# Optimization experiments

Hardware: AMD Instinct MI355X
Metric: run time of the kernel (lower is better)

## Reference

```python
import jax, jax.numpy as jnp
import numpy as np

A = 4096          # agents
N_OBJ = 8192      # objects
IN_DIM = 16       # input_dim
EMBED = 128       # embedding_dim
MAX_OBJ = 16      # max set size
DEG = 8           # communicate in-degree (constant, target-major edges)
OBS_DEG = 8       # observe degree
POS_DIM = 2
ORIG = IN_DIM + POS_DIM   # 18, decoded element dim
THRES = 0.02              # duplicate filter distance threshold


def setup_inputs() -> dict:
    key = jax.random.key(0)
    ks = jax.random.split(key, 16)
    def lin(k, fi, fo):
        return (jax.random.normal(k, (fi, fo), jnp.float32) / np.float32(np.sqrt(fi)))
    obj_x = jax.random.normal(ks[0], (N_OBJ, IN_DIM), jnp.float32)
    obj_pos = jax.random.uniform(ks[1], (N_OBJ, POS_DIM), jnp.float32) * 10.0
    agent_pos = jax.random.uniform(ks[2], (A, POS_DIM), jnp.float32) * 10.0
    # (agent, observe, object) edges: row0 = agent, row1 = object (as in the torch HeteroData)
    obs_tgt = jnp.repeat(jnp.arange(A), OBS_DEG)
    obs_src = jax.random.randint(ks[3], (A * OBS_DEG,), 0, N_OBJ)
    obs_edge_index = jnp.stack([obs_tgt, obs_src])
    # (agent, communicate, agent) edges: row0 = source j, row1 = target i; target-major, constant degree
    tgt = jnp.repeat(jnp.arange(A), DEG)
    src = (tgt + 1 + jnp.tile(jnp.arange(DEG), A)) % A
    comm_edge_index = jnp.stack([src, tgt])
    return dict(
        obj_x=obj_x, obj_pos=obj_pos, agent_pos=agent_pos,
        enc_W1=lin(ks[4], ORIG, EMBED), enc_b1=jnp.zeros((EMBED,), jnp.float32),
        enc_W2=lin(ks[5], EMBED, EMBED), enc_b2=jnp.zeros((EMBED,), jnp.float32),
        mdec_Ws=lin(ks[6], EMBED, MAX_OBJ + 1), mdec_bs=jnp.zeros((MAX_OBJ + 1,), jnp.float32),
        mdec_Wx=lin(ks[7], EMBED, MAX_OBJ * ORIG), mdec_bx=jnp.zeros((MAX_OBJ * ORIG,), jnp.float32),
        menc_W1=lin(ks[8], ORIG, EMBED), menc_b1=jnp.zeros((EMBED,), jnp.float32),
        menc_W2=lin(ks[9], EMBED, EMBED), menc_b2=jnp.zeros((EMBED,), jnp.float32),
        dec_Ws=lin(ks[10], EMBED, MAX_OBJ + 1), dec_bs=jnp.zeros((MAX_OBJ + 1,), jnp.float32),
        dec_Wx=lin(ks[11], EMBED, MAX_OBJ * ORIG), dec_bx=jnp.zeros((MAX_OBJ * ORIG,), jnp.float32),
        obs_edge_index=obs_edge_index, comm_edge_index=comm_edge_index,
    )


def reference(obj_x, obj_pos, agent_pos,
              enc_W1, enc_b1, enc_W2, enc_b2,
              mdec_Ws, mdec_bs, mdec_Wx, mdec_bx,
              menc_W1, menc_b1, menc_W2, menc_b2,
              dec_Ws, dec_bs, dec_Wx, dec_bx,
              obs_edge_index, comm_edge_index):
    nA = agent_pos.shape[0]
    # ---- EncodeGNN: edge_index.flip -> source = object (row1), target = agent (row0)
    o = obs_edge_index[1]
    a = obs_edge_index[0]
    # message: [x_j, posx_j - posa_i] (position='rel')
    msg = jnp.concatenate([obj_x[o], obj_pos[o] - agent_pos[a]], axis=-1)      # [E_obs, ORIG]
    h = jax.nn.relu(msg @ enc_W1 + enc_b1)
    enc = jax.ops.segment_sum(h, a, num_segments=nA) @ enc_W2 + enc_b2         # [A, EMBED]
    # ---- MergeGNN message: decode source embedding per communicate edge
    j = comm_edge_index[0]
    i = comm_edge_index[1]
    zj = enc[j]                                                                 # [E, EMBED]
    npred = jnp.argmax(zj @ mdec_Ws + mdec_bs, axis=-1)                         # predicted set size per edge
    elems = (zj @ mdec_Wx + mdec_bx).reshape(-1, MAX_OBJ, ORIG)                 # [E, MAX_OBJ, ORIG]
    # update_rel_pos: decoded_pos += pos_j - pos_i
    relpos = (agent_pos[j] - agent_pos[i])[:, None, :]
    elems = jnp.concatenate([elems[..., :-POS_DIM], elems[..., -POS_DIM:] + relpos], axis=-1)
    valid = jnp.arange(MAX_OBJ)[None, :] < npred[:, None]                       # [E, MAX_OBJ]
    # ---- aggregate: edges are target-major with constant degree -> per-agent candidate pool
    deg = comm_edge_index.shape[1] // nA
    K = deg * MAX_OBJ
    cand = elems.reshape(nA, K, ORIG)
    v = valid.reshape(nA, K)
    # filter_duplicates (pos_only=True): pairwise distance on last POS_DIM dims
    pos = cand[..., -POS_DIM:]
    D = jnp.linalg.norm(pos[:, :, None, :] - pos[:, None, :, :], axis=-1)       # [A, K, K]
    tri = jnp.triu(jnp.ones((K, K), bool), k=1)
    dup = (D < THRES) & tri[None] & v[:, :, None] & v[:, None, :]
    keep = v & ~jnp.any(dup, axis=1)                                            # column is dup of an earlier row
    cnt = jnp.cumsum(keep.astype(jnp.int32), axis=1)
    keep = keep & (cnt <= MAX_OBJ - 1)                                          # cap at max_n - 1 kept elements
    # merge_encoder: masked set encode per agent
    hm = jax.nn.relu(cand @ menc_W1 + menc_b1) * keep[..., None]
    merged = hm.sum(axis=1) @ menc_W2 + menc_b2                                 # [A, EMBED]
    # ---- final decoder
    n2 = jnp.argmax(merged @ dec_Ws + dec_bs, axis=-1)
    decoded = (merged @ dec_Wx + dec_bx).reshape(nA, MAX_OBJ, ORIG)
    mask = jnp.arange(MAX_OBJ)[None, :] < n2[:, None]
    decoded = decoded * mask[..., None]                                         # padded+masked ragged set
    batch = jnp.broadcast_to(jnp.arange(nA)[:, None], (nA, MAX_OBJ))
    return decoded, batch, mask
```

## Files before the change

### kernel.cpp

```cpp
#include <hip/hip_runtime.h>

#define A_N   4096
#define EMBED 128
#define MAXO  16
#define DEG   8
#define OBSD  8
#define ORIG  18
#define KCAND 128
#define G     4
#define NBLK  (A_N / G)
#define NTHR  256

__global__ __launch_bounds__(NTHR) void enc4_kernel(
    const float* __restrict__ obj_x, const float* __restrict__ obj_pos,
    const float* __restrict__ agent_pos,
    const float* __restrict__ enc_W1, const float* __restrict__ enc_b1,
    const float* __restrict__ enc_W2, const float* __restrict__ enc_b2,
    const float* __restrict__ mdec_Ws, const float* __restrict__ mdec_bs,
    const float* __restrict__ mdec_Wx, const float* __restrict__ mdec_bx,
    const int* __restrict__ obs_edge,
    float* __restrict__ elems_base, int* __restrict__ npred_out)
{
    const int blk = blockIdx.x, tid = threadIdx.x;
    const int i0  = blk * G;
    const int col = tid & 127, pair = tid >> 7;

    __shared__ int    on[G][OBSD];
    __shared__ float  msg[G * OBSD][20];
    __shared__ float4 SG[EMBED];
    __shared__ float4 Ep[2][EMBED];
    __shared__ float4 Eg[EMBED];
    __shared__ float  lgts[G][MAXO + 1];

    if (tid < G * OBSD) {
        const int g = tid >> 3, d = tid & 7;
        on[g][d] = obs_edge[A_N * OBSD + (i0 + g) * OBSD + d];
    }
    __syncthreads();
    for (int idx = tid; idx < G * OBSD * ORIG; idx += NTHR) {
        const int r = idx / ORIG, c = idx % ORIG;
        const int g = r >> 3, d = r & 7;
        const int o = on[g][d];
        float v;
        if (c < 16) v = obj_x[o * 16 + c];
        else        v = obj_pos[o * 2 + (c - 16)] - agent_pos[(i0 + g) * 2 + (c - 16)];
        msg[r][c] = v;
    }
    __syncthreads();

    {
        float w1[ORIG];
#pragma unroll
        for (int c = 0; c < ORIG; ++c) w1[c] = enc_W1[c * EMBED + col];
        const float b1 = enc_b1[col];
#pragma unroll
        for (int gg = 0; gg < 2; ++gg) {
            const int g = 2 * pair + gg;
            float acc = 0.f;
#pragma unroll
            for (int d = 0; d < OBSD; ++d) {
                const int r = g * OBSD + d;
                const float4* mr = (const float4*)&msg[r][0];
                const float4 m0 = mr[0], m1 = mr[1], m2 = mr[2], m3 = mr[3];
                const float2 m4 = *(const float2*)&msg[r][16];
                float h = b1
                    + m0.x*w1[0]  + m0.y*w1[1]  + m0.z*w1[2]  + m0.w*w1[3]
                    + m1.x*w1[4]  + m1.y*w1[5]  + m1.z*w1[6]  + m1.w*w1[7]
                    + m2.x*w1[8]  + m2.y*w1[9]  + m2.z*w1[10] + m2.w*w1[11]
                    + m3.x*w1[12] + m3.y*w1[13] + m3.z*w1[14] + m3.w*w1[15]
                    + m4.x*w1[16] + m4.y*w1[17];
                acc += fmaxf(h, 0.f);
            }
            ((float*)&SG[col])[g] = acc;
        }
    }
    __syncthreads();

    {
        float4 acc = {0.f, 0.f, 0.f, 0.f};
        const int c0 = 64 * pair;
#pragma unroll 8
        for (int c = c0; c < c0 + 64; ++c) {
            const float4 s = SG[c];
            const float  w = enc_W2[c * EMBED + col];
            acc.x += s.x * w; acc.y += s.y * w; acc.z += s.z * w; acc.w += s.w * w;
        }
        Ep[pair][col] = acc;
    }
    __syncthreads();
    if (tid < EMBED) {
        const float4 a = Ep[0][tid], b = Ep[1][tid];
        const float bb = enc_b2[tid];
        float4 e;
        e.x = a.x + b.x + bb; e.y = a.y + b.y + bb;
        e.z = a.z + b.z + bb; e.w = a.w + b.w + bb;
        Eg[tid] = e;
    }
    __syncthreads();

    if (tid < G * (MAXO + 1)) {
        const int g = tid / (MAXO + 1), q = tid % (MAXO + 1);
        float v = mdec_bs[q];
        for (int c = 0; c < EMBED; ++c)
            v += ((const float*)&Eg[c])[g] * mdec_Ws[c * (MAXO + 1) + q];
        lgts[g][q] = v;
    }
    __syncthreads();
    if (tid < G) {
        int best = 0; float bv = lgts[tid][0];
        for (int q = 1; q <= MAXO; ++q) if (lgts[tid][q] > bv) { bv = lgts[tid][q]; best = q; }
        npred_out[i0 + tid] = best;
    }

    for (int e = tid; e < MAXO * ORIG; e += NTHR) {
        const float bx = mdec_bx[e];
        float4 acc = {bx, bx, bx, bx};
#pragma unroll 8
        for (int c = 0; c < EMBED; ++c) {
            const float4 s = Eg[c];
            const float  w = mdec_Wx[c * (MAXO * ORIG) + e];
            acc.x += s.x * w; acc.y += s.y * w; acc.z += s.z * w; acc.w += s.w * w;
        }
        elems_base[(size_t)(i0 + 0) * (MAXO * ORIG) + e] = acc.x;
        elems_base[(size_t)(i0 + 1) * (MAXO * ORIG) + e] = acc.y;
        elems_base[(size_t)(i0 + 2) * (MAXO * ORIG) + e] = acc.z;
        elems_base[(size_t)(i0 + 3) * (MAXO * ORIG) + e] = acc.w;
    }
}

__global__ __launch_bounds__(NTHR) void merge4_kernel(
    const float* __restrict__ agent_pos,
    const float* __restrict__ menc_W1, const float* __restrict__ menc_b1,
    const float* __restrict__ menc_W2, const float* __restrict__ menc_b2,
    const float* __restrict__ dec_Ws, const float* __restrict__ dec_bs,
    const float* __restrict__ dec_Wx, const float* __restrict__ dec_bx,
    const int* __restrict__ comm_edge,
    const float* __restrict__ elems_base, const int* __restrict__ npred,
    float* __restrict__ out_dec, float* __restrict__ out_batch,
    float* __restrict__ out_mask)
{
    const int blk = blockIdx.x, tid = threadIdx.x;
    const int i0  = blk * G;
    const int col = tid & 127, pair = tid >> 7;
    const int lane = tid & 63, wv = tid >> 6;

    __shared__ int    jn[G][DEG];
    __shared__ float  relx[G][DEG], rely[G][DEG];
    __shared__ int    npd[G][DEG];
    __shared__ float2 pxy[G][KCAND];
    __shared__ int    vl[G][KCAND];
    __shared__ int    nvp[G], nv[G];
    __shared__ int    kpp[G], kcnt[G];
    __shared__ int    klist[G][MAXO];
    __shared__ float  kc[G][MAXO][20];
    __shared__ float4 Hs[EMBED];
    __shared__ float4 Mp[2][EMBED];
    __shared__ float4 Mg[EMBED];
    __shared__ float  lg2[G][MAXO + 1];
    __shared__ int    n2s[G];

    if (tid < G * DEG) {
        const int g = tid >> 3, d = tid & 7;
        const int e = (i0 + g) * DEG + d;
        const int j  = comm_edge[e];
        const int ii = comm_edge[A_N * DEG + e];
        jn[g][d]  = j;
        relx[g][d] = agent_pos[j * 2 + 0] - agent_pos[ii * 2 + 0];
        rely[g][d] = agent_pos[j * 2 + 1] - agent_pos[ii * 2 + 1];
        npd[g][d] = npred[j];
    }
    __syncthreads();

    for (int r = 0; r < 2; ++r) {
        const int k = 64 * r + lane;
        const int d = k >> 4, m = k & 15;
        const float* eb = elems_base + (size_t)jn[wv][d] * (MAXO * ORIG) + m * ORIG;
        float2 p = *(const float2*)(eb + 16);
        p.x += relx[wv][d]; p.y += rely[wv][d];
        pxy[wv][k] = p;
        const int val = (m < npd[wv][d]) ? 1 : 0;
        const unsigned long long bal = __ballot(val);
        const int pref = (int)__popcll(bal << (63 - lane));
        const int base = (r == 0) ? 0 : nvp[wv];
        if (val) vl[wv][base + pref - 1] = k;
        if (lane == 63) {
            if (r == 0) nvp[wv] = (int)__popcll(bal);
            else        nv[wv]  = nvp[wv] + (int)__popcll(bal);
        }
    }

    for (int r = 0; r < 2; ++r) {
        const int k = 64 * r + lane;
        const float2 my = pxy[wv][k];
        const int nvg = nv[wv];
        int dup = 0;
        for (int idx = 0; idx < nvg; ++idx) {
            const int k1 = vl[wv][idx];
            if (k1 >= k) break;
            const float2 p1 = pxy[wv][k1];
            const float dx = p1.x - my.x, dy = p1.y - my.y;
            if (sqrtf(dx * dx + dy * dy) < 0.02f) dup = 1;
        }
        const int val = ((k & 15) < npd[wv][k >> 4]) ? 1 : 0;
        const int kp = (val && !dup) ? 1 : 0;
        const unsigned long long bal = __ballot(kp);
        const int pref = (int)__popcll(bal << (63 - lane));
        const int base = (r == 0) ? 0 : kpp[wv];
        const int cnt = base + pref;
        if (kp && cnt <= MAXO - 1) klist[wv][cnt - 1] = k;
        if (lane == 63) {
            if (r == 0) kpp[wv] = (int)__popcll(bal);
            else {
                int tot = kpp[wv] + (int)__popcll(bal);
                kcnt[wv] = (tot < MAXO - 1) ? tot : (MAXO - 1);
            }
        }
    }
    __syncthreads();

    for (int idx = tid; idx < G * MAXO * ORIG; idx += NTHR) {
        const int g = idx / (MAXO * ORIG), rem = idx % (MAXO * ORIG);
        const int s = rem / ORIG, c = rem % ORIG;
        if (s < kcnt[g]) {
            const int k = klist[g][s], d = k >> 4, m = k & 15;
            float v;
            if (c < 16) v = elems_base[(size_t)jn[g][d] * (MAXO * ORIG) + m * ORIG + c];
            else        v = (c == 16) ? pxy[g][k].x : pxy[g][k].y;
            kc[g][s][c] = v;
        }
    }
    __syncthreads();

    {
        float w1[ORIG];
#pragma unroll
        for (int c = 0; c < ORIG; ++c) w1[c] = menc_W1[c * EMBED + col];
        const float b1 = menc_b1[col];
#pragma unroll
        for (int gg = 0; gg < 2; ++gg) {
            const int g = 2 * pair + gg;
            const int nk = kcnt[g];
            float hs = 0.f;
            for (int s = 0; s < nk; ++s) {
                const float4* mr = (const float4*)&kc[g][s][0];
                const float4 m0 = mr[0], m1 = mr[1], m2 = mr[2], m3 = mr[3];
                const float2 m4 = *(const float2*)&kc[g][s][16];
                float h = b1
                    + m0.x*w1[0]  + m0.y*w1[1]  + m0.z*w1[2]  + m0.w*w1[3]
                    + m1.x*w1[4]  + m1.y*w1[5]  + m1.z*w1[6]  + m1.w*w1[7]
                    + m2.x*w1[8]  + m2.y*w1[9]  + m2.z*w1[10] + m2.w*w1[11]
                    + m3.x*w1[12] + m3.y*w1[13] + m3.z*w1[14] + m3.w*w1[15]
                    + m4.x*w1[16] + m4.y*w1[17];
                hs += fmaxf(h, 0.f);
            }
            ((float*)&Hs[col])[g] = hs;
        }
    }
    __syncthreads();

    {
        float4 acc = {0.f, 0.f, 0.f, 0.f};
        const int c0 = 64 * pair;
#pragma unroll 8
        for (int c = c0; c < c0 + 64; ++c) {
            const float4 s = Hs[c];
            const float  w = menc_W2[c * EMBED + col];
            acc.x += s.x * w; acc.y += s.y * w; acc.z += s.z * w; acc.w += s.w * w;
        }
        Mp[pair][col] = acc;
    }
    __syncthreads();
    if (tid < EMBED) {
        const float4 a = Mp[0][tid], b = Mp[1][tid];
        const float bb = menc_b2[tid];
        float4 e;
        e.x = a.x + b.x + bb; e.y = a.y + b.y + bb;
        e.z = a.z + b.z + bb; e.w = a.w + b.w + bb;
        Mg[tid] = e;
    }
    __syncthreads();

    if (tid < G * (MAXO + 1)) {
        const int g = tid / (MAXO + 1), q = tid % (MAXO + 1);
        float v = dec_bs[q];
        for (int c = 0; c < EMBED; ++c)
            v += ((const float*)&Mg[c])[g] * dec_Ws[c * (MAXO + 1) + q];
        lg2[g][q] = v;
    }
    __syncthreads();
    if (tid < G) {
        int best = 0; float bv = lg2[tid][0];
        for (int q = 1; q <= MAXO; ++q) if (lg2[tid][q] > bv) { bv = lg2[tid][q]; best = q; }
        n2s[tid] = best;
    }
    __syncthreads();

    for (int e = tid; e < MAXO * ORIG; e += NTHR) {
        const int m = e / ORIG;
        const float bx = dec_bx[e];
        float4 acc = {bx, bx, bx, bx};
#pragma unroll 8
        for (int c = 0; c < EMBED; ++c) {
            const float4 s = Mg[c];
            const float  w = dec_Wx[c * (MAXO * ORIG) + e];
            acc.x += s.x * w; acc.y += s.y * w; acc.z += s.z * w; acc.w += s.w * w;
        }
        out_dec[(size_t)(i0 + 0) * (MAXO * ORIG) + e] = (m < n2s[0]) ? acc.x : 0.f;
        out_dec[(size_t)(i0 + 1) * (MAXO * ORIG) + e] = (m < n2s[1]) ? acc.y : 0.f;
        out_dec[(size_t)(i0 + 2) * (MAXO * ORIG) + e] = (m < n2s[2]) ? acc.z : 0.f;
        out_dec[(size_t)(i0 + 3) * (MAXO * ORIG) + e] = (m < n2s[3]) ? acc.w : 0.f;
    }
    if (tid < G * MAXO) {
        const int g = tid >> 4, m = tid & 15;
        out_batch[(i0 + g) * MAXO + m] = (float)(i0 + g);
        out_mask[(i0 + g) * MAXO + m]  = (m < n2s[g]) ? 1.f : 0.f;
    }
}

extern "C" void kernel_launch(void* const* d_in, const int* in_sizes, int n_in,
                              void* d_out, int out_size, void* d_ws, size_t ws_size,
                              hipStream_t stream)
{
    const float* obj_x     = (const float*)d_in[0];
    const float* obj_pos   = (const float*)d_in[1];
    const float* agent_pos = (const float*)d_in[2];
    const float* enc_W1    = (const float*)d_in[3];
    const float* enc_b1    = (const float*)d_in[4];
    const float* enc_W2    = (const float*)d_in[5];
    const float* enc_b2    = (const float*)d_in[6];
    const float* mdec_Ws   = (const float*)d_in[7];
    const float* mdec_bs   = (const float*)d_in[8];
    const float* mdec_Wx   = (const float*)d_in[9];
    const float* mdec_bx   = (const float*)d_in[10];
    const float* menc_W1   = (const float*)d_in[11];
    const float* menc_b1   = (const float*)d_in[12];
    const float* menc_W2   = (const float*)d_in[13];
    const float* menc_b2   = (const float*)d_in[14];
    const float* dec_Ws    = (const float*)d_in[15];
    const float* dec_bs    = (const float*)d_in[16];
    const float* dec_Wx    = (const float*)d_in[17];
    const float* dec_bx    = (const float*)d_in[18];
    const int*   obs_edge  = (const int*)d_in[19];
    const int*   comm_edge = (const int*)d_in[20];

    float* elems_base = (float*)d_ws;
    int*   npred      = (int*)((char*)d_ws + (size_t)A_N * MAXO * ORIG * sizeof(float));

    float* out_dec   = (float*)d_out;
    float* out_batch = out_dec + (size_t)A_N * MAXO * ORIG;
    float* out_mask  = out_batch + (size_t)A_N * MAXO;

    enc4_kernel<<<NBLK, NTHR, 0, stream>>>(
        obj_x, obj_pos, agent_pos, enc_W1, enc_b1, enc_W2, enc_b2,
        mdec_Ws, mdec_bs, mdec_Wx, mdec_bx, obs_edge, elems_base, npred);

    merge4_kernel<<<NBLK, NTHR, 0, stream>>>(
        agent_pos, menc_W1, menc_b1, menc_W2, menc_b2,
        dec_Ws, dec_bs, dec_Wx, dec_bx, comm_edge,
        elems_base, npred, out_dec, out_batch, out_mask);
}
```

Measured before the change: 176.7 us.

## Double block threads to 512 and split-K the decoder and encoder GEMVs

Raises threads per block from 256 to 512 in both kernels. Each 128-thread group now handles one agent in the first layer, the second layer splits its K range four ways, and the 288-wide decode GEMV splits K in two with partials reduced through shared memory. The per-agent dedup scan now uses two waves per agent, joined by block barriers, instead of one wave looping twice. The aim is more parallel work per block and a shorter serial decode loop, at the cost of extra barriers, more shared memory and a reduction step.

Result: faster. 163.9 us (-7.3%).

```diff
diff --git a/kernel.cpp b/kernel.cpp
--- a/kernel.cpp
+++ b/kernel.cpp
@@ -9,9 +9,10 @@
 #define KCAND 128
 #define G     4
 #define NBLK  (A_N / G)
-#define NTHR  256
-
-__global__ __launch_bounds__(NTHR) void enc4_kernel(
+#define NTHR  512
+#define EL    (MAXO * ORIG)
+
+__global__ __launch_bounds__(NTHR, 8) void enc512_kernel(
     const float* __restrict__ obj_x, const float* __restrict__ obj_pos,
     const float* __restrict__ agent_pos,
     const float* __restrict__ enc_W1, const float* __restrict__ enc_b1,
@@ -23,14 +24,15 @@
 {
     const int blk = blockIdx.x, tid = threadIdx.x;
     const int i0  = blk * G;
-    const int col = tid & 127, pair = tid >> 7;
+    const int col = tid & 127, q = tid >> 7;
 
     __shared__ int    on[G][OBSD];
     __shared__ float  msg[G * OBSD][20];
     __shared__ float4 SG[EMBED];
-    __shared__ float4 Ep[2][EMBED];
+    __shared__ float4 Ep4[4][EMBED];
     __shared__ float4 Eg[EMBED];
     __shared__ float  lgts[G][MAXO + 1];
+    __shared__ float4 Pp[2][EL];
 
     if (tid < G * OBSD) {
         const int g = tid >> 3, d = tid & 7;
@@ -53,82 +55,94 @@
 #pragma unroll
         for (int c = 0; c < ORIG; ++c) w1[c] = enc_W1[c * EMBED + col];
         const float b1 = enc_b1[col];
+        float acc = 0.f;
 #pragma unroll
-        for (int gg = 0; gg < 2; ++gg) {
-            const int g = 2 * pair + gg;
-            float acc = 0.f;
-#pragma unroll
-            for (int d = 0; d < OBSD; ++d) {
-                const int r = g * OBSD + d;
-                const float4* mr = (const float4*)&msg[r][0];
-                const float4 m0 = mr[0], m1 = mr[1], m2 = mr[2], m3 = mr[3];
-                const float2 m4 = *(const float2*)&msg[r][16];
-                float h = b1
-                    + m0.x*w1[0]  + m0.y*w1[1]  + m0.z*w1[2]  + m0.w*w1[3]
-                    + m1.x*w1[4]  + m1.y*w1[5]  + m1.z*w1[6]  + m1.w*w1[7]
-                    + m2.x*w1[8]  + m2.y*w1[9]  + m2.z*w1[10] + m2.w*w1[11]
-                    + m3.x*w1[12] + m3.y*w1[13] + m3.z*w1[14] + m3.w*w1[15]
-                    + m4.x*w1[16] + m4.y*w1[17];
-                acc += fmaxf(h, 0.f);
-            }
-            ((float*)&SG[col])[g] = acc;
-        }
+        for (int d = 0; d < OBSD; ++d) {
+            const int r = q * OBSD + d;
+            const float4* mr = (const float4*)&msg[r][0];
+            const float4 m0 = mr[0], m1 = mr[1], m2 = mr[2], m3 = mr[3];
+            const float2 m4 = *(const float2*)&msg[r][16];
+            float h = b1
+                + m0.x*w1[0]  + m0.y*w1[1]  + m0.z*w1[2]  + m0.w*w1[3]
+                + m1.x*w1[4]  + m1.y*w1[5]  + m1.z*w1[6]  + m1.w*w1[7]
+                + m2.x*w1[8]  + m2.y*w1[9]  + m2.z*w1[10] + m2.w*w1[11]
+                + m3.x*w1[12] + m3.y*w1[13] + m3.z*w1[14] + m3.w*w1[15]
+                + m4.x*w1[16] + m4.y*w1[17];
+            acc += fmaxf(h, 0.f);
+        }
+        ((float*)&SG[col])[q] = acc;
     }
     __syncthreads();
 
     {
         float4 acc = {0.f, 0.f, 0.f, 0.f};
-        const int c0 = 64 * pair;
+        const int c0 = 32 * q;
 #pragma unroll 8
-        for (int c = c0; c < c0 + 64; ++c) {
+        for (int c = c0; c < c0 + 32; ++c) {
             const float4 s = SG[c];
             const float  w = enc_W2[c * EMBED + col];
             acc.x += s.x * w; acc.y += s.y * w; acc.z += s.z * w; acc.w += s.w * w;
         }
-        Ep[pair][col] = acc;
+        Ep4[q][col] = acc;
     }
     __syncthreads();
     if (tid < EMBED) {
-        const float4 a = Ep[0][tid], b = Ep[1][tid];
+        const float4 a = Ep4[0][tid], b = Ep4[1][tid], c = Ep4[2][tid], d = Ep4[3][tid];
         const float bb = enc_b2[tid];
         float4 e;
-        e.x = a.x + b.x + bb; e.y = a.y + b.y + bb;
-        e.z = a.z + b.z + bb; e.w = a.w + b.w + bb;
+        e.x = a.x + b.x + c.x + d.x + bb;
+        e.y = a.y + b.y + c.y + d.y + bb;
+        e.z = a.z + b.z + c.z + d.z + bb;
+        e.w = a.w + b.w + c.w + d.w + bb;
         Eg[tid] = e;
     }
     __syncthreads();
 
     if (tid < G * (MAXO + 1)) {
-        const int g = tid / (MAXO + 1), q = tid % (MAXO + 1);
-        float v = mdec_bs[q];
+        const int g = tid / (MAXO + 1), qq = tid % (MAXO + 1);
+        float v = mdec_bs[qq];
         for (int c = 0; c < EMBED; ++c)
-            v += ((const float*)&Eg[c])[g] * mdec_Ws[c * (MAXO + 1) + q];
-        lgts[g][q] = v;
+            v += ((const float*)&Eg[c])[g] * mdec_Ws[c * (MAXO + 1) + qq];
+        lgts[g][qq] = v;
     }
     __syncthreads();
     if (tid < G) {
         int best = 0; float bv = lgts[tid][0];
-        for (int q = 1; q <= MAXO; ++q) if (lgts[tid][q] > bv) { bv = lgts[tid][q]; best = q; }
+        for (int qq = 1; qq <= MAXO; ++qq) if (lgts[tid][qq] > bv) { bv = lgts[tid][qq]; best = qq; }
         npred_out[i0 + tid] = best;
     }
 
-    for (int e = tid; e < MAXO * ORIG; e += NTHR) {
-        const float bx = mdec_bx[e];
-        float4 acc = {bx, bx, bx, bx};
+    {
+        int u = tid;
+        for (int pass = 0; pass < 2; ++pass) {
+            if (u < 2 * EL) {
+                const int h = (u >= EL) ? 1 : 0;
+                const int e = u - h * EL;
+                float4 acc = {0.f, 0.f, 0.f, 0.f};
+                const int c0 = 64 * h;
 #pragma unroll 8
-        for (int c = 0; c < EMBED; ++c) {
-            const float4 s = Eg[c];
-            const float  w = mdec_Wx[c * (MAXO * ORIG) + e];
-            acc.x += s.x * w; acc.y += s.y * w; acc.z += s.z * w; acc.w += s.w * w;
-        }
-        elems_base[(size_t)(i0 + 0) * (MAXO * ORIG) + e] = acc.x;
-        elems_base[(size_t)(i0 + 1) * (MAXO * ORIG) + e] = acc.y;
-        elems_base[(size_t)(i0 + 2) * (MAXO * ORIG) + e] = acc.z;
-        elems_base[(size_t)(i0 + 3) * (MAXO * ORIG) + e] = acc.w;
+                for (int c = c0; c < c0 + 64; ++c) {
+                    const float4 s = Eg[c];
+                    const float  w = mdec_Wx[c * EL + e];
+                    acc.x += s.x * w; acc.y += s.y * w; acc.z += s.z * w; acc.w += s.w * w;
+                }
+                Pp[h][e] = acc;
+            }
+            u = NTHR + tid;
+        }
+    }
+    __syncthreads();
+    if (tid < EL) {
+        const float4 a = Pp[0][tid], b = Pp[1][tid];
+        const float bx = mdec_bx[tid];
+        elems_base[(size_t)(i0 + 0) * EL + tid] = a.x + b.x + bx;
+        elems_base[(size_t)(i0 + 1) * EL + tid] = a.y + b.y + bx;
+        elems_base[(size_t)(i0 + 2) * EL + tid] = a.z + b.z + bx;
+        elems_base[(size_t)(i0 + 3) * EL + tid] = a.w + b.w + bx;
     }
 }
 
-__global__ __launch_bounds__(NTHR) void merge4_kernel(
+__global__ __launch_bounds__(NTHR, 8) void merge512_kernel(
     const float* __restrict__ agent_pos,
     const float* __restrict__ menc_W1, const float* __restrict__ menc_b1,
     const float* __restrict__ menc_W2, const float* __restrict__ menc_b2,
@@ -141,23 +155,25 @@
 {
     const int blk = blockIdx.x, tid = threadIdx.x;
     const int i0  = blk * G;
-    const int col = tid & 127, pair = tid >> 7;
+    const int col = tid & 127, q = tid >> 7;
     const int lane = tid & 63, wv = tid >> 6;
+    const int w = wv >> 1, half = wv & 1;
 
     __shared__ int    jn[G][DEG];
     __shared__ float  relx[G][DEG], rely[G][DEG];
     __shared__ int    npd[G][DEG];
     __shared__ float2 pxy[G][KCAND];
     __shared__ int    vl[G][KCAND];
-    __shared__ int    nvp[G], nv[G];
-    __shared__ int    kpp[G], kcnt[G];
+    __shared__ int    wcv[G][2], kcv[G][2];
+    __shared__ int    nv[G], kcnt[G];
     __shared__ int    klist[G][MAXO];
     __shared__ float  kc[G][MAXO][20];
     __shared__ float4 Hs[EMBED];
-    __shared__ float4 Mp[2][EMBED];
+    __shared__ float4 Mp4[4][EMBED];
     __shared__ float4 Mg[EMBED];
     __shared__ float  lg2[G][MAXO + 1];
     __shared__ int    n2s[G];
+    __shared__ float4 Pp[2][EL];
 
     if (tid < G * DEG) {
         const int g = tid >> 3, d = tid & 7;
@@ -171,61 +187,58 @@
     }
     __syncthreads();
 
-    for (int r = 0; r < 2; ++r) {
-        const int k = 64 * r + lane;
-        const int d = k >> 4, m = k & 15;
-        const float* eb = elems_base + (size_t)jn[wv][d] * (MAXO * ORIG) + m * ORIG;
+    const int k = 64 * half + lane;
+    const int kd = k >> 4, km = k & 15;
+    {
+        const float* eb = elems_base + (size_t)jn[w][kd] * EL + km * ORIG;
         float2 p = *(const float2*)(eb + 16);
-        p.x += relx[wv][d]; p.y += rely[wv][d];
-        pxy[wv][k] = p;
-        const int val = (m < npd[wv][d]) ? 1 : 0;
+        p.x += relx[w][kd]; p.y += rely[w][kd];
+        pxy[w][k] = p;
+        const int val = (km < npd[w][kd]) ? 1 : 0;
         const unsigned long long bal = __ballot(val);
         const int pref = (int)__popcll(bal << (63 - lane));
-        const int base = (r == 0) ? 0 : nvp[wv];
-        if (val) vl[wv][base + pref - 1] = k;
-        if (lane == 63) {
-            if (r == 0) nvp[wv] = (int)__popcll(bal);
-            else        nv[wv]  = nvp[wv] + (int)__popcll(bal);
-        }
-    }
-
-    for (int r = 0; r < 2; ++r) {
-        const int k = 64 * r + lane;
-        const float2 my = pxy[wv][k];
-        const int nvg = nv[wv];
+        if (lane == 63) wcv[w][half] = (int)__popcll(bal);
+        __syncthreads();
+        const int base = half ? wcv[w][0] : 0;
+        if (val) vl[w][base + pref - 1] = k;
+        if (lane == 0 && half == 0) nv[w] = wcv[w][0] + wcv[w][1];
+        __syncthreads();
+    }
+
+    {
+        const float2 my = pxy[w][k];
+        const int nvg = nv[w];
         int dup = 0;
         for (int idx = 0; idx < nvg; ++idx) {
-            const int k1 = vl[wv][idx];
+            const int k1 = vl[w][idx];
             if (k1 >= k) break;
-            const float2 p1 = pxy[wv][k1];
+            const float2 p1 = pxy[w][k1];
             const float dx = p1.x - my.x, dy = p1.y - my.y;
             if (sqrtf(dx * dx + dy * dy) < 0.02f) dup = 1;
         }
-        const int val = ((k & 15) < npd[wv][k >> 4]) ? 1 : 0;
+        const int val = (km < npd[w][kd]) ? 1 : 0;
         const int kp = (val && !dup) ? 1 : 0;
         const unsigned long long bal = __ballot(kp);
         const int pref = (int)__popcll(bal << (63 - lane));
-        const int base = (r == 0) ? 0 : kpp[wv];
-        const int cnt = base + pref;
-        if (kp && cnt <= MAXO - 1) klist[wv][cnt - 1] = k;
-        if (lane == 63) {
-            if (r == 0) kpp[wv] = (int)__popcll(bal);
-            else {
-                int tot = kpp[wv] + (int)__popcll(bal);
-                kcnt[wv] = (tot < MAXO - 1) ? tot : (MAXO - 1);
-            }
-        }
-    }
-    __syncthreads();
-
-    for (int idx = tid; idx < G * MAXO * ORIG; idx += NTHR) {
-        const int g = idx / (MAXO * ORIG), rem = idx % (MAXO * ORIG);
+        if (lane == 63) kcv[w][half] = (int)__popcll(bal);
+        __syncthreads();
+        const int cnt = (half ? kcv[w][0] : 0) + pref;
+        if (kp && cnt <= MAXO - 1) klist[w][cnt - 1] = k;
+        if (lane == 0 && half == 0) {
+            const int tot = kcv[w][0] + kcv[w][1];
+            kcnt[w] = (tot < MAXO - 1) ? tot : (MAXO - 1);
+        }
+        __syncthreads();
+    }
+
+    for (int idx = tid; idx < G * EL; idx += NTHR) {
+        const int g = idx / EL, rem = idx % EL;
         const int s = rem / ORIG, c = rem % ORIG;
         if (s < kcnt[g]) {
-            const int k = klist[g][s], d = k >> 4, m = k & 15;
+            const int kk = klist[g][s], d = kk >> 4, m = kk & 15;
             float v;
-            if (c < 16) v = elems_base[(size_t)jn[g][d] * (MAXO * ORIG) + m * ORIG + c];
-            else        v = (c == 16) ? pxy[g][k].x : pxy[g][k].y;
+            if (c < 16) v = elems_base[(size_t)jn[g][d] * EL + m * ORIG + c];
+            else        v = (c == 16) ? pxy[g][kk].x : pxy[g][kk].y;
             kc[g][s][c] = v;
         }
     }
@@ -236,82 +249,94 @@
 #pragma unroll
         for (int c = 0; c < ORIG; ++c) w1[c] = menc_W1[c * EMBED + col];
         const float b1 = menc_b1[col];
-#pragma unroll
-        for (int gg = 0; gg < 2; ++gg) {
-            const int g = 2 * pair + gg;
-            const int nk = kcnt[g];
-            float hs = 0.f;
-            for (int s = 0; s < nk; ++s) {
-                const float4* mr = (const float4*)&kc[g][s][0];
-                const float4 m0 = mr[0], m1 = mr[1], m2 = mr[2], m3 = mr[3];
-                const float2 m4 = *(const float2*)&kc[g][s][16];
-                float h = b1
-                    + m0.x*w1[0]  + m0.y*w1[1]  + m0.z*w1[2]  + m0.w*w1[3]
-                    + m1.x*w1[4]  + m1.y*w1[5]  + m1.z*w1[6]  + m1.w*w1[7]
-                    + m2.x*w1[8]  + m2.y*w1[9]  + m2.z*w1[10] + m2.w*w1[11]
-                    + m3.x*w1[12] + m3.y*w1[13] + m3.z*w1[14] + m3.w*w1[15]
-                    + m4.x*w1[16] + m4.y*w1[17];
-                hs += fmaxf(h, 0.f);
-            }
-            ((float*)&Hs[col])[g] = hs;
-        }
+        const int nk = kcnt[q];
+        float hs = 0.f;
+        for (int s = 0; s < nk; ++s) {
+            const float4* mr = (const float4*)&kc[q][s][0];
+            const float4 m0 = mr[0], m1 = mr[1], m2 = mr[2], m3 = mr[3];
+            const float2 m4 = *(const float2*)&kc[q][s][16];
+            float h = b1
+                + m0.x*w1[0]  + m0.y*w1[1]  + m0.z*w1[2]  + m0.w*w1[3]
+                + m1.x*w1[4]  + m1.y*w1[5]  + m1.z*w1[6]  + m1.w*w1[7]
+                + m2.x*w1[8]  + m2.y*w1[9]  + m2.z*w1[10] + m2.w*w1[11]
+                + m3.x*w1[12] + m3.y*w1[13] + m3.z*w1[14] + m3.w*w1[15]
+                + m4.x*w1[16] + m4.y*w1[17];
+            hs += fmaxf(h, 0.f);
+        }
+        ((float*)&Hs[col])[q] = hs;
     }
     __syncthreads();
 
     {
         float4 acc = {0.f, 0.f, 0.f, 0.f};
-        const int c0 = 64 * pair;
+        const int c0 = 32 * q;
 #pragma unroll 8
-        for (int c = c0; c < c0 + 64; ++c) {
+        for (int c = c0; c < c0 + 32; ++c) {
             const float4 s = Hs[c];
-            const float  w = menc_W2[c * EMBED + col];
-            acc.x += s.x * w; acc.y += s.y * w; acc.z += s.z * w; acc.w += s.w * w;
-        }
-        Mp[pair][col] = acc;
+            const float  ww = menc_W2[c * EMBED + col];
+            acc.x += s.x * ww; acc.y += s.y * ww; acc.z += s.z * ww; acc.w += s.w * ww;
+        }
+        Mp4[q][col] = acc;
     }
     __syncthreads();
     if (tid < EMBED) {
-        const float4 a = Mp[0][tid], b = Mp[1][tid];
+        const float4 a = Mp4[0][tid], b = Mp4[1][tid], c = Mp4[2][tid], d = Mp4[3][tid];
         const float bb = menc_b2[tid];
         float4 e;
-        e.x = a.x + b.x + bb; e.y = a.y + b.y + bb;
-        e.z = a.z + b.z + bb; e.w = a.w + b.w + bb;
+        e.x = a.x + b.x + c.x + d.x + bb;
+        e.y = a.y + b.y + c.y + d.y + bb;
+        e.z = a.z + b.z + c.z + d.z + bb;
+        e.w = a.w + b.w + c.w + d.w + bb;
         Mg[tid] = e;
     }
     __syncthreads();
 
     if (tid < G * (MAXO + 1)) {
-        const int g = tid / (MAXO + 1), q = tid % (MAXO + 1);
-        float v = dec_bs[q];
+        const int g = tid / (MAXO + 1), qq = tid % (MAXO + 1);
+        float v = dec_bs[qq];
         for (int c = 0; c < EMBED; ++c)
-            v += ((const float*)&Mg[c])[g] * dec_Ws[c * (MAXO + 1) + q];
-        lg2[g][q] = v;
+            v += ((const float*)&Mg[c])[g] * dec_Ws[c * (MAXO + 1) + qq];
+        lg2[g][qq] = v;
     }
     __syncthreads();
     if (tid < G) {
         int best = 0; float bv = lg2[tid][0];
-        for (int q = 1; q <= MAXO; ++q) if (lg2[tid][q] > bv) { bv = lg2[tid][q]; best = q; }
+        for (int qq = 1; qq <= MAXO; ++qq) if (lg2[tid][qq] > bv) { bv = lg2[tid][qq]; best = qq; }
         n2s[tid] = best;
     }
     __syncthreads();
 
-    for (int e = tid; e < MAXO * ORIG; e += NTHR) {
-        const int m = e / ORIG;
-        const float bx = dec_bx[e];
-        float4 acc = {bx, bx, bx, bx};
+    {
+        int u = tid;
+        for (int pass = 0; pass < 2; ++pass) {
+            if (u < 2 * EL) {
+                const int h = (u >= EL) ? 1 : 0;
+                const int e = u - h * EL;
+                float4 acc = {0.f, 0.f, 0.f, 0.f};
+                const int c0 = 64 * h;
 #pragma unroll 8
-        for (int c = 0; c < EMBED; ++c) {
-            const float4 s = Mg[c];
-            const float  w = dec_Wx[c * (MAXO * ORIG) + e];
-            acc.x += s.x * w; acc.y += s.y * w; acc.z += s.z * w; acc.w += s.w * w;
-        }
-        out_dec[(size_t)(i0 + 0) * (MAXO * ORIG) + e] = (m < n2s[0]) ? acc.x : 0.f;
-        out_dec[(size_t)(i0 + 1) * (MAXO * ORIG) + e] = (m < n2s[1]) ? acc.y : 0.f;
-        out_dec[(size_t)(i0 + 2) * (MAXO * ORIG) + e] = (m < n2s[2]) ? acc.z : 0.f;
-        out_dec[(size_t)(i0 + 3) * (MAXO * ORIG) + e] = (m < n2s[3]) ? acc.w : 0.f;
-    }
-    if (tid < G * MAXO) {
-        const int g = tid >> 4, m = tid & 15;
+                for (int c = c0; c < c0 + 64; ++c) {
+                    const float4 s = Mg[c];
+                    const float  ww = dec_Wx[c * EL + e];
+                    acc.x += s.x * ww; acc.y += s.y * ww; acc.z += s.z * ww; acc.w += s.w * ww;
+                }
+                Pp[h][e] = acc;
+            }
+            u = NTHR + tid;
+        }
+    }
+    __syncthreads();
+    if (tid < EL) {
+        const int m = tid / ORIG;
+        const float4 a = Pp[0][tid], b = Pp[1][tid];
+        const float bx = dec_bx[tid];
+        out_dec[(size_t)(i0 + 0) * EL + tid] = (m < n2s[0]) ? (a.x + b.x + bx) : 0.f;
+        out_dec[(size_t)(i0 + 1) * EL + tid] = (m < n2s[1]) ? (a.y + b.y + bx) : 0.f;
+        out_dec[(size_t)(i0 + 2) * EL + tid] = (m < n2s[2]) ? (a.z + b.z + bx) : 0.f;
+        out_dec[(size_t)(i0 + 3) * EL + tid] = (m < n2s[3]) ? (a.w + b.w + bx) : 0.f;
+    } else if (tid >= NTHR - G * MAXO) {
+        const int idx = tid - (NTHR - G * MAXO);
+        const int g = idx >> 4, m = idx & 15;
         out_batch[(i0 + g) * MAXO + m] = (float)(i0 + g);
         out_mask[(i0 + g) * MAXO + m]  = (m < n2s[g]) ? 1.f : 0.f;
     }
@@ -344,17 +369,17 @@
     const int*   comm_edge = (const int*)d_in[20];
 
     float* elems_base = (float*)d_ws;
-    int*   npred      = (int*)((char*)d_ws + (size_t)A_N * MAXO * ORIG * sizeof(float));
+    int*   npred      = (int*)((char*)d_ws + (size_t)A_N * EL * sizeof(float));
 
     float* out_dec   = (float*)d_out;
-    float* out_batch = out_dec + (size_t)A_N * MAXO * ORIG;
+    float* out_batch = out_dec + (size_t)A_N * EL;
     float* out_mask  = out_batch + (size_t)A_N * MAXO;
 
-    enc4_kernel<<<NBLK, NTHR, 0, stream>>>(
+    enc512_kernel<<<NBLK, NTHR, 0, stream>>>(
         obj_x, obj_pos, agent_pos, enc_W1, enc_b1, enc_W2, enc_b2,
         mdec_Ws, mdec_bs, mdec_Wx, mdec_bx, obs_edge, elems_base, npred);
 
-    merge4_kernel<<<NBLK, NTHR, 0, stream>>>(
+    merge512_kernel<<<NBLK, NTHR, 0, stream>>>(
         agent_pos, menc_W1, menc_b1, menc_W2, menc_b2,
         dec_Ws, dec_bs, dec_Wx, dec_bx, comm_edge,
         elems_base, npred, out_dec, out_batch, out_mask);
```
